# Optimization experiments

Measured on AMD Instinct MI355X. Metric: run time of the kernel, lower is better.

The kernel has to match this reference:

```python
import jax, jax.numpy as jnp
import numpy as np

N_SIDE = 7
N_NODES = N_SIDE * N_SIDE  # 49


def _grid_edge_index(h, w):
    # torch_geometric.utils.grid: 9-point stencil (8 neighbors + self-loop)
    src, dst = [], []
    for y in range(h):
        for x in range(w):
            for dy in (-1, 0, 1):
                for dx in (-1, 0, 1):
                    ny, nx = y + dy, x + dx
                    if 0 <= ny < h and 0 <= nx < w:
                        src.append(ny * w + nx)
                        dst.append(y * w + x)
    return np.stack([np.array(src), np.array(dst)]).astype(np.int64)


def _gcn_norm_adj(edge_index, n):
    # PyG GCNConv default: add self-loops (on top of any existing), weight 1,
    # deg = in-degree by edge weight, A_hat = D^-1/2 (A + I) D^-1/2
    src, dst = edge_index[0], edge_index[1]
    A = jnp.zeros((n, n), dtype=jnp.float32).at[dst, src].add(1.0)
    A = A + jnp.eye(n, dtype=jnp.float32)  # GCNConv's added self-loops
    deg = A.sum(axis=1)
    d_inv_sqrt = jnp.where(deg > 0, jax.lax.rsqrt(deg), 0.0)
    return A * d_inv_sqrt[:, None] * d_inv_sqrt[None, :]  # [n, n]


def setup_inputs() -> dict:
    key = jax.random.key(0)
    ks = jax.random.split(key, 4)
    B = 4096
    features = jax.random.normal(ks[0], (B, N_NODES, 768), dtype=jnp.float32)
    W1 = jax.random.normal(ks[1], (768, 256), dtype=jnp.float32) * (1.0 / np.sqrt(768))
    b1 = jnp.zeros((256,), dtype=jnp.float32)
    W2 = jax.random.normal(ks[2], (256, 128), dtype=jnp.float32) * (1.0 / np.sqrt(256))
    b2 = jnp.zeros((128,), dtype=jnp.float32)
    fcW = jax.random.normal(ks[3], (128, 4), dtype=jnp.float32) * (1.0 / np.sqrt(128))
    fcb = jnp.zeros((4,), dtype=jnp.float32)
    edge_index = jnp.asarray(_grid_edge_index(N_SIDE, N_SIDE))  # [2, 361]
    return {"features": features, "W1": W1, "b1": b1, "W2": W2, "b2": b2,
            "fcW": fcW, "fcb": fcb, "edge_index": edge_index}


def reference(features, W1, b1, W2, b2, fcW, fcb, edge_index):
    # features: [B, N, 768]; batched GCN over the shared 7x7 grid graph
    A_hat = _gcn_norm_adj(edge_index, N_NODES)  # [N, N]
    # GCNConv: aggregate(X @ W) + b
    h = jnp.einsum('mn,bnd->bmd', A_hat, features @ W1) + b1  # [B, N, 256]
    h = jax.nn.relu(h)
    h = jnp.einsum('mn,bnd->bmd', A_hat, h @ W2) + b2  # [B, N, 128]
    h = jax.nn.relu(h)
    pooled = h.mean(axis=1)  # [B, 128] mean over nodes
    return pooled @ fcW + fcb  # [B, 4]
```

## Files before the change

kernel.cpp:

```cpp
#include <hip/hip_runtime.h>

#define NN 49
#define D0 768
#define D1 256
#define D2 128

typedef short v8s __attribute__((ext_vector_type(8)));
typedef float v4f __attribute__((ext_vector_type(4)));
typedef int   v4i __attribute__((ext_vector_type(4)));

__device__ __forceinline__ unsigned short f2bf(float f) {
  unsigned int u = __float_as_uint(f);
  u += 0x7FFFu + ((u >> 16) & 1u);
  return (unsigned short)(u >> 16);
}
__device__ __forceinline__ float bf2f(unsigned short u) {
  return __uint_as_float((unsigned)u << 16);
}

__device__ __forceinline__ int permk(int k) {
  return (k & ~31) | ((k & 12) << 1) | ((k & 16) >> 2) | (k & 3);
}

__device__ __forceinline__ float ahat(int m, int k) {
  if (m >= NN || k >= NN) return 0.f;
  int ym = m / 7, xm = m % 7, yk = k / 7, xk = k % 7;
  int dy = ym - yk, dx = xm - xk;
  if (dy < -1 || dy > 1 || dx < -1 || dx > 1) return 0.f;
  float rm = rsqrtf((float)((1 + (ym > 0) + (ym < 6)) * (1 + (xm > 0) + (xm < 6))) + 1.0f);
  float rk = rsqrtf((float)((1 + (yk > 0) + (yk < 6)) * (1 + (xk > 0) + (xk < 6))) + 1.0f);
  return ((m == k) ? 2.0f : 1.0f) * rm * rk;
}

#define W1_IMG_BYTES 393216
#define AH_OFF       458752
#define WS_NEEDED    524288

__global__ void prep_w(const float* __restrict__ W1, const float* __restrict__ W2,
                       char* __restrict__ wimg) {
  int id = blockIdx.x * 256 + threadIdx.x;
  if (id < 24576) {
    int p = (id >> 8) & 7, tt = id & 255;
    int wvv = tt >> 6, lnn = tt & 63, qq = lnn >> 4, lmm = lnn & 15;
    int nt = p >> 1, s = p & 1;
    int n  = 64 * wvv + 16 * nt + lmm;
    int k0 = (id >> 11) * 64 + 32 * s + 4 * qq;
    v8s v;
    #pragma unroll
    for (int i = 0; i < 4; ++i) {
      v[i]     = (short)f2bf(W1[(size_t)(k0 + i) * D1 + n]);
      v[i + 4] = (short)f2bf(W1[(size_t)(k0 + 16 + i) * D1 + n]);
    }
    *(v8s*)(wimg + (size_t)id * 16) = v;
  }
  int id2 = id - 24576;
  if (id2 >= 0 && id2 < 4096) {
    int p = (id2 >> 8) & 3, tt = id2 & 255;
    int wvv = tt >> 6, lnn = tt & 63, qq = lnn >> 4, lmm = lnn & 15;
    int nt = p >> 1, s = p & 1;
    int n  = 32 * wvv + 16 * nt + lmm;
    int k0 = (id2 >> 10) * 64 + 32 * s + 4 * qq;
    v8s v;
    #pragma unroll
    for (int i = 0; i < 4; ++i) {
      v[i]     = (short)f2bf(W2[(size_t)(k0 + i) * D2 + n]);
      v[i + 4] = (short)f2bf(W2[(size_t)(k0 + 16 + i) * D2 + n]);
    }
    *(v8s*)(wimg + W1_IMG_BYTES + (size_t)id2 * 16) = v;
  }
  int id3 = id - 28672;
  if (id3 >= 0 && id3 < 2048) {
    int tt = id3 & 255, ms = id3 >> 8;
    int mt = ms >> 1, s2 = ms & 1;
    int lnn = tt & 63, qq = lnn >> 4, lmm = lnn & 15;
    int m = 16 * mt + lmm;
    v8s hi, lo;
    #pragma unroll
    for (int j = 0; j < 8; ++j) {
      int k = 32 * s2 + ((j & 4) << 2) + 4 * qq + (j & 3);
      float v = ahat(m, k);
      unsigned short h = f2bf(v);
      hi[j] = (short)h;
      lo[j] = (short)f2bf(v - bf2f(h));
    }
    *(v8s*)(wimg + AH_OFF + (size_t)id3 * 16) = hi;
    *(v8s*)(wimg + AH_OFF + 32768 + (size_t)id3 * 16) = lo;
  }
}

#define SX0    0
#define SX1    8192
#define SH1_0  16384
#define SH1_1  49152
#define SPOOL0 0
#define SPOOL1 512
#define NSMEM7 81920

__device__ __forceinline__ void ldw8(v8s* dst, const char* base) {
  #pragma unroll
  for (int p = 0; p < 8; ++p) dst[p] = *(const v8s*)(base + p * 4096);
}
__device__ __forceinline__ void ldw4(v8s* dst, const char* base) {
  #pragma unroll
  for (int p = 0; p < 4; ++p) dst[p] = *(const v8s*)(base + p * 4096);
}
__device__ __forceinline__ void commit8(char* lds, const float4& a, const float4& b) {
  v8s v;
  v[0] = (short)f2bf(a.x); v[1] = (short)f2bf(a.y);
  v[2] = (short)f2bf(a.z); v[3] = (short)f2bf(a.w);
  v[4] = (short)f2bf(b.x); v[5] = (short)f2bf(b.y);
  v[6] = (short)f2bf(b.z); v[7] = (short)f2bf(b.w);
  *(v8s*)lds = v;
}

__global__ __launch_bounds__(256, 2) void gcn_fused10(
    const float* __restrict__ X, const char* __restrict__ wimg,
    const float* __restrict__ b1v, const float* __restrict__ b2v,
    const float* __restrict__ fcWv, const float* __restrict__ fcbv,
    float* __restrict__ out)
{
  __shared__ __align__(16) char smem[NSMEM7];
  const int t  = threadIdx.x;
  const int wv = t >> 6;
  const int ln = t & 63;
  const int q  = ln >> 4;
  const int lm = ln & 15;

  if (t < 240) {
    int i = (t >= 120) ? t - 120 : t;
    int base = ((t >= 120) ? SX1 : SX0) + 6272 + i * 16;
    *(v4i*)(smem + base) = (v4i){0, 0, 0, 0};
  }

  const float* X0 = X + (size_t)(2 * blockIdx.x) * (NN * D0);
  const float* X1 = X0 + NN * D0;

  const int g1 = t + 256;
  const int b1g = (g1 >= 392) ? 1 : 0;
  const bool act3 = (t < 16);
  const int s0 = t, s1 = g1 - 392 * b1g, s2 = t + 120, s3 = t + 376;
  const int r0 = s0 >> 3, f0 = s0 & 7;
  const int r1 = s1 >> 3, f1 = s1 & 7;
  const int r2 = s2 >> 3, f2 = s2 & 7;
  const int r3 = s3 >> 3, f3 = s3 & 7;
  const float* base0 = X0 + r0 * D0 + 32 * (f0 >> 2) + 4 * (f0 & 3);
  const float* base1 = (b1g ? X1 : X0) + r1 * D0 + 32 * (f1 >> 2) + 4 * (f1 & 3);
  const float* base2 = X1 + r2 * D0 + 32 * (f2 >> 2) + 4 * (f2 & 3);
  const float* base3_ = X1 + r3 * D0 + 32 * (f3 >> 2) + 4 * (f3 & 3);
  const float* base3 = act3 ? base3_ : base0;
  const int lds0 = SX0 + ((r0 * 128 + 16 * f0) ^ ((r0 & 7) << 4));
  const int lds1 = (b1g ? SX1 : SX0) + ((r1 * 128 + 16 * f1) ^ ((r1 & 7) << 4));
  const int lds2 = SX1 + ((r2 * 128 + 16 * f2) ^ ((r2 & 7) << 4));
  const int lds3 = SX1 + (((r3 & 63) * 128 + 16 * f3) ^ ((r3 & 7) << 4));

  const int tofs = t * 16;

  v4f accA[4][4], accB[4][4];
  #pragma unroll
  for (int i = 0; i < 4; ++i)
    #pragma unroll
    for (int j = 0; j < 4; ++j) {
      accA[i][j] = (v4f){0.f, 0.f, 0.f, 0.f};
      accB[i][j] = (v4f){0.f, 0.f, 0.f, 0.f};
    }

  v8s wA[8];
  ldw8(wA, wimg + tofs);
  float4 p0a = *(const float4*)(base0);
  float4 p0b = *(const float4*)(base0 + 16);
  float4 p1a = *(const float4*)(base1);
  float4 p1b = *(const float4*)(base1 + 16);
  float4 p2a = *(const float4*)(base2);
  float4 p2b = *(const float4*)(base2 + 16);
  float4 p3a = *(const float4*)(base3);
  float4 p3b = *(const float4*)(base3 + 16);

  for (int kc = 0; kc < 12; ++kc) {
    __builtin_amdgcn_sched_barrier(0);
    __builtin_amdgcn_s_barrier();
    __builtin_amdgcn_sched_barrier(0);
    commit8((char*)smem + lds0, p0a, p0b);
    commit8((char*)smem + lds1, p1a, p1b);
    commit8((char*)smem + lds2, p2a, p2b);
    if (act3) commit8((char*)smem + lds3, p3a, p3b);
    if (kc < 11) {
      const int o = (kc + 1) * 64;
      p0a = *(const float4*)(base0 + o);
      p0b = *(const float4*)(base0 + o + 16);
      p1a = *(const float4*)(base1 + o);
      p1b = *(const float4*)(base1 + o + 16);
      p2a = *(const float4*)(base2 + o);
      p2b = *(const float4*)(base2 + o + 16);
      p3a = *(const float4*)(base3 + o);
      p3b = *(const float4*)(base3 + o + 16);
    }
    __builtin_amdgcn_sched_barrier(0);
    asm volatile("s_waitcnt lgkmcnt(0)" ::: "memory");
    __builtin_amdgcn_s_barrier();
    __builtin_amdgcn_sched_barrier(0);
    #pragma unroll
    for (int ks = 0; ks < 2; ++ks) {
      const int off = ks * 64 + (q << 4);
      v8s af[4];
      #pragma unroll
      for (int mt = 0; mt < 4; ++mt) {
        int row = mt * 16 + lm;
        af[mt] = *(const v8s*)(smem + SX0 + ((row * 128 + off) ^ ((row & 7) << 4)));
      }
      #pragma unroll
      for (int mt = 0; mt < 4; ++mt)
        #pragma unroll
        for (int nt = 0; nt < 4; ++nt)
          accA[mt][nt] = __builtin_amdgcn_mfma_f32_16x16x32_bf16(af[mt], wA[2 * nt + ks], accA[mt][nt], 0, 0, 0);
    }
    #pragma unroll
    for (int ks = 0; ks < 2; ++ks) {
      const int off = ks * 64 + (q << 4);
      v8s af[4];
      #pragma unroll
      for (int mt = 0; mt < 4; ++mt) {
        int row = mt * 16 + lm;
        af[mt] = *(const v8s*)(smem + SX1 + ((row * 128 + off) ^ ((row & 7) << 4)));
      }
      #pragma unroll
      for (int mt = 0; mt < 4; ++mt)
        #pragma unroll
        for (int nt = 0; nt < 4; ++nt)
          accB[mt][nt] = __builtin_amdgcn_mfma_f32_16x16x32_bf16(af[mt], wA[2 * nt + ks], accB[mt][nt], 0, 0, 0);
    }
    if (kc < 11) ldw8(wA, wimg + (kc + 1) * 32768 + tofs);
  }

  const char* ahimg = wimg + AH_OFF;
  v8s afH[4][2], afL[4][2];
  #pragma unroll
  for (int mt = 0; mt < 4; ++mt)
    #pragma unroll
    for (int s2 = 0; s2 < 2; ++s2) {
      const int idx = ((mt * 2 + s2) * 256 + t) * 16;
      afH[mt][s2] = *(const v8s*)(ahimg + idx);
      afL[mt][s2] = *(const v8s*)(ahimg + 32768 + idx);
    }

  v8s bA[2][4], bB[2][4];
  #pragma unroll
  for (int s2 = 0; s2 < 2; ++s2)
    #pragma unroll
    for (int nt = 0; nt < 4; ++nt) {
      v8s a, b;
      #pragma unroll
      for (int i = 0; i < 4; ++i) {
        a[i]     = (short)f2bf(accA[2 * s2][nt][i]);
        a[i + 4] = (short)f2bf(accA[2 * s2 + 1][nt][i]);
        b[i]     = (short)f2bf(accB[2 * s2][nt][i]);
        b[i + 4] = (short)f2bf(accB[2 * s2 + 1][nt][i]);
      }
      bA[s2][nt] = a; bB[s2][nt] = b;
    }

  float bi[4];
  #pragma unroll
  for (int nt = 0; nt < 4; ++nt) bi[nt] = b1v[64 * wv + 16 * nt + lm];

  #pragma unroll
  for (int bb = 0; bb < 2; ++bb) {
    v4f ag[4][4];
    #pragma unroll
    for (int mt = 0; mt < 4; ++mt)
      #pragma unroll
      for (int nt = 0; nt < 4; ++nt)
        ag[mt][nt] = (v4f){bi[nt], bi[nt], bi[nt], bi[nt]};
    #pragma unroll
    for (int s2 = 0; s2 < 2; ++s2)
      #pragma unroll
      for (int nt = 0; nt < 4; ++nt) {
        v8s b = (bb == 0) ? bA[s2][nt] : bB[s2][nt];
        #pragma unroll
        for (int mt = 0; mt < 4; ++mt) {
          ag[mt][nt] = __builtin_amdgcn_mfma_f32_16x16x32_bf16(afL[mt][s2], b, ag[mt][nt], 0, 0, 0);
          ag[mt][nt] = __builtin_amdgcn_mfma_f32_16x16x32_bf16(afH[mt][s2], b, ag[mt][nt], 0, 0, 0);
        }
      }
    const int hbase = (bb == 0) ? SH1_0 : SH1_1;
    #pragma unroll
    for (int mt = 0; mt < 4; ++mt)
      #pragma unroll
      for (int nt = 0; nt < 4; ++nt) {
        int ch  = 64 * wv + 16 * nt + lm;
        int chb = 2 * permk(ch);
        #pragma unroll
        for (int r = 0; r < 4; ++r) {
          int row = 16 * mt + 4 * q + r;
          float hv = fmaxf(ag[mt][nt][r], 0.f);
          int byte = (row * 512 + chb) ^ ((row & 7) << 4);
          *(unsigned short*)(smem + hbase + byte) = f2bf(hv);
        }
      }
  }

  const char* w2img = wimg + W1_IMG_BYTES;
  v8s w2c0[4], w2c1[4], w2c2[4], w2c3[4];
  ldw4(w2c0, w2img + tofs);
  ldw4(w2c1, w2img + 16384 + tofs);
  ldw4(w2c2, w2img + 2 * 16384 + tofs);
  ldw4(w2c3, w2img + 3 * 16384 + tofs);

  __builtin_amdgcn_sched_barrier(0);
  asm volatile("s_waitcnt lgkmcnt(0)" ::: "memory");
  __builtin_amdgcn_s_barrier();
  __builtin_amdgcn_sched_barrier(0);

  float b2i0 = b2v[32 * wv + lm];
  float b2i1 = b2v[32 * wv + 16 + lm];

  #pragma unroll
  for (int bb = 0; bb < 2; ++bb) {
    const int hbase = (bb == 0) ? SH1_0 : SH1_1;
    v4f acc3[4][2];
    #pragma unroll
    for (int i = 0; i < 4; ++i) {
      acc3[i][0] = (v4f){0.f, 0.f, 0.f, 0.f};
      acc3[i][1] = (v4f){0.f, 0.f, 0.f, 0.f};
    }
    #pragma unroll
    for (int kc = 0; kc < 4; ++kc)
      #pragma unroll
      for (int ks = 0; ks < 2; ++ks) {
        const int off = ks * 64 + (q << 4);
        v8s af[4];
        #pragma unroll
        for (int mt = 0; mt < 4; ++mt) {
          int row = mt * 16 + lm;
          int byte = (row * 512 + kc * 128 + off) ^ ((row & 7) << 4);
          af[mt] = *(const v8s*)(smem + hbase + byte);
        }
        const v8s* wc = (kc == 0) ? w2c0 : (kc == 1) ? w2c1 : (kc == 2) ? w2c2 : w2c3;
        #pragma unroll
        for (int mt = 0; mt < 4; ++mt)
          #pragma unroll
          for (int nt = 0; nt < 2; ++nt)
            acc3[mt][nt] = __builtin_amdgcn_mfma_f32_16x16x32_bf16(af[mt], wc[2 * nt + ks], acc3[mt][nt], 0, 0, 0);
      }
    v4f a2[4][2];
    #pragma unroll
    for (int mt = 0; mt < 4; ++mt) {
      a2[mt][0] = (v4f){b2i0, b2i0, b2i0, b2i0};
      a2[mt][1] = (v4f){b2i1, b2i1, b2i1, b2i1};
    }
    #pragma unroll
    for (int s2 = 0; s2 < 2; ++s2)
      #pragma unroll
      for (int nt = 0; nt < 2; ++nt) {
        v8s b;
        #pragma unroll
        for (int i = 0; i < 4; ++i) {
          b[i]     = (short)f2bf(acc3[2 * s2][nt][i]);
          b[i + 4] = (short)f2bf(acc3[2 * s2 + 1][nt][i]);
        }
        #pragma unroll
        for (int mt = 0; mt < 4; ++mt) {
          a2[mt][nt] = __builtin_amdgcn_mfma_f32_16x16x32_bf16(afL[mt][s2], b, a2[mt][nt], 0, 0, 0);
          a2[mt][nt] = __builtin_amdgcn_mfma_f32_16x16x32_bf16(afH[mt][s2], b, a2[mt][nt], 0, 0, 0);
        }
      }
    float ps0 = 0.f, ps1 = 0.f;
    #pragma unroll
    for (int mt = 0; mt < 3; ++mt)
      #pragma unroll
      for (int r = 0; r < 4; ++r) {
        ps0 += fmaxf(a2[mt][0][r], 0.f);
        ps1 += fmaxf(a2[mt][1][r], 0.f);
      }
    if (q == 0) {
      ps0 += fmaxf(a2[3][0][0], 0.f);
      ps1 += fmaxf(a2[3][1][0], 0.f);
    }
    ps0 += __shfl_xor(ps0, 16); ps0 += __shfl_xor(ps0, 32);
    ps1 += __shfl_xor(ps1, 16); ps1 += __shfl_xor(ps1, 32);
    float* spool = (float*)(smem + ((bb == 0) ? SPOOL0 : SPOOL1));
    if (q == 0) {
      spool[32 * wv + lm]      = ps0 * (1.0f / 49.0f);
      spool[32 * wv + 16 + lm] = ps1 * (1.0f / 49.0f);
    }
  }
  __syncthreads();
  {
    const int bb = wv >> 1;
    const int c0 = (wv & 1) * 2;
    const float* spool = (const float*)(smem + (bb ? SPOOL1 : SPOOL0));
    float d0 = spool[ln];
    float d1 = spool[ln + 64];
    float a0 = d0 * fcWv[ln * 4 + c0]     + d1 * fcWv[(ln + 64) * 4 + c0];
    float a1 = d0 * fcWv[ln * 4 + c0 + 1] + d1 * fcWv[(ln + 64) * 4 + c0 + 1];
    #pragma unroll
    for (int s = 32; s; s >>= 1) { a0 += __shfl_xor(a0, s); a1 += __shfl_xor(a1, s); }
    if (ln == 0) {
      out[(size_t)(2 * blockIdx.x + bb) * 4 + c0]     = a0 + fcbv[c0];
      out[(size_t)(2 * blockIdx.x + bb) * 4 + c0 + 1] = a1 + fcbv[c0 + 1];
    }
  }
}

#define OFF_SX    0
#define OFF_SWT   8192
#define OFF_SC    0
#define OFF_SWT2  0
#define OFF_SPOOL 25872
#define OFF_SPF   30096
#define OFF_SH1   40960
#define OFF_NBRW  73728
#define OFF_NBRI  75492
#define OFF_B1    77256
#define OFF_B2    78280
#define OFF_FCW   78792
#define OFF_FCB   80840
#define SMEM_SZ   80856

__global__ __launch_bounds__(256, 2) void gcn_fused_fb(
    const float* __restrict__ X, const float* __restrict__ W1,
    const float* __restrict__ b1v, const float* __restrict__ W2,
    const float* __restrict__ b2v, const float* __restrict__ fcWv,
    const float* __restrict__ fcbv, float* __restrict__ out)
{
  __shared__ __align__(16) char smem[SMEM_SZ];
  const int t  = threadIdx.x;
  const int wv = t >> 6;
  const int ln = t & 63;
  const int q  = ln >> 4;
  const int lm = ln & 15;

  float* nbrW = (float*)(smem + OFF_NBRW);
  int*   nbrI = (int*)  (smem + OFF_NBRI);
  float* b1s  = (float*)(smem + OFF_B1);
  float* b2s  = (float*)(smem + OFF_B2);
  float* fcWs = (float*)(smem + OFF_FCW);
  float* fcbs = (float*)(smem + OFF_FCB);
  float* sC   = (float*)(smem + OFF_SC);

  if (t < D1) b1s[t] = b1v[t];
  if (t < D2) b2s[t] = b2v[t];
  fcWs[t]       = fcWv[t];
  fcWs[t + 256] = fcWv[t + 256];
  if (t < 4) fcbs[t] = fcbv[t];
  if (t < NN) {
    int y = t / 7, x = t % 7;
    float rm = rsqrtf((float)((1 + (y > 0) + (y < 6)) * (1 + (x > 0) + (x < 6))) + 1.0f);
    int cnt = 0;
    for (int dy = -1; dy <= 1; ++dy)
      for (int dx = -1; dx <= 1; ++dx) {
        int ny = y + dy, nx = x + dx;
        if (ny >= 0 && ny < 7 && nx >= 0 && nx < 7) {
          int n = ny * 7 + nx;
          float rn = rsqrtf((float)((1 + (ny > 0) + (ny < 6)) * (1 + (nx > 0) + (nx < 6))) + 1.0f);
          nbrW[t * 9 + cnt] = ((n == t) ? 2.0f : 1.0f) * rm * rn;
          nbrI[t * 9 + cnt] = n;
          ++cnt;
        }
      }
    for (; cnt < 9; ++cnt) { nbrW[t * 9 + cnt] = 0.0f; nbrI[t * 9 + cnt] = 0; }
  }
  __syncthreads();

  const float* Xb = X + (size_t)blockIdx.x * (NN * D0);
  v4f acc[4][4];
  #pragma unroll
  for (int i = 0; i < 4; ++i)
    #pragma unroll
    for (int j = 0; j < 4; ++j)
      acc[i][j] = (v4f){0.f, 0.f, 0.f, 0.f};

  for (int kc = 0; kc < 12; ++kc) {
    __syncthreads();
    #pragma unroll
    for (int p = 0; p < 4; ++p) {
      int idx = t + 256 * p;
      int row = idx >> 4;
      int k4  = (idx & 15) << 2;
      float4 v = {0.f, 0.f, 0.f, 0.f};
      if (row < NN) v = *(const float4*)(Xb + row * D0 + kc * 64 + k4);
      ushort4 s;
      s.x = f2bf(v.x); s.y = f2bf(v.y); s.z = f2bf(v.z); s.w = f2bf(v.w);
      int byte = row * 128 + 2 * permk(k4);
      byte ^= (row & 7) << 4;
      *(ushort4*)(smem + OFF_SX + byte) = s;
    }
    #pragma unroll
    for (int p = 0; p < 4; ++p) {
      int bid2 = t + 256 * p;
      int k0 = (bid2 & 15) << 2;
      int n0 = (bid2 >> 4) << 2;
      const float* wp = W1 + (size_t)(kc * 64 + k0) * D1 + n0;
      float4 r0 = *(const float4*)(wp);
      float4 r1 = *(const float4*)(wp + D1);
      float4 r2 = *(const float4*)(wp + 2 * D1);
      float4 r3 = *(const float4*)(wp + 3 * D1);
      int kb = 2 * permk(k0);
      ushort4 s; int byte;
      s.x = f2bf(r0.x); s.y = f2bf(r1.x); s.z = f2bf(r2.x); s.w = f2bf(r3.x);
      byte = (n0 + 0) * 128 + kb; byte ^= ((n0 + 0) & 7) << 4;
      *(ushort4*)(smem + OFF_SWT + byte) = s;
      s.x = f2bf(r0.y); s.y = f2bf(r1.y); s.z = f2bf(r2.y); s.w = f2bf(r3.y);
      byte = (n0 + 1) * 128 + kb; byte ^= ((n0 + 1) & 7) << 4;
      *(ushort4*)(smem + OFF_SWT + byte) = s;
      s.x = f2bf(r0.z); s.y = f2bf(r1.z); s.z = f2bf(r2.z); s.w = f2bf(r3.z);
      byte = (n0 + 2) * 128 + kb; byte ^= ((n0 + 2) & 7) << 4;
      *(ushort4*)(smem + OFF_SWT + byte) = s;
      s.x = f2bf(r0.w); s.y = f2bf(r1.w); s.z = f2bf(r2.w); s.w = f2bf(r3.w);
      byte = (n0 + 3) * 128 + kb; byte ^= ((n0 + 3) & 7) << 4;
      *(ushort4*)(smem + OFF_SWT + byte) = s;
    }
    __syncthreads();
    #pragma unroll
    for (int ks = 0; ks < 2; ++ks) {
      int off = ks * 64 + (q << 4);
      v8s af[4], bf[4];
      #pragma unroll
      for (int mt = 0; mt < 4; ++mt) {
        int row = mt * 16 + lm;
        int byte = row * 128 + off; byte ^= (row & 7) << 4;
        af[mt] = *(const v8s*)(smem + OFF_SX + byte);
      }
      #pragma unroll
      for (int nt = 0; nt < 4; ++nt) {
        int n = (wv * 4 + nt) * 16 + lm;
        int byte = n * 128 + off; byte ^= (n & 7) << 4;
        bf[nt] = *(const v8s*)(smem + OFF_SWT + byte);
      }
      #pragma unroll
      for (int mt = 0; mt < 4; ++mt)
        #pragma unroll
        for (int nt = 0; nt < 4; ++nt)
          acc[mt][nt] = __builtin_amdgcn_mfma_f32_16x16x32_bf16(af[mt], bf[nt], acc[mt][nt], 0, 0, 0);
    }
  }

  #pragma unroll
  for (int h = 0; h < 2; ++h) {
    __syncthreads();
    if ((wv >> 1) == h) {
      #pragma unroll
      for (int mt = 0; mt < 4; ++mt) {
        int rbase = mt * 16 + (q << 2);
        #pragma unroll
        for (int nt = 0; nt < 4; ++nt) {
          int c = ((wv & 1) * 4 + nt) * 16 + lm;
          #pragma unroll
          for (int r = 0; r < 4; ++r) {
            int row = rbase + r;
            if (row < NN) sC[row * 132 + c] = acc[mt][nt][r];
          }
        }
      }
    }
    __syncthreads();
    for (int p = 0; p < 7; ++p) {
      int idx = t + 256 * p;
      if (idx < NN * 32) {
        int m  = idx >> 5;
        int d4 = (idx & 31) << 2;
        int dg = h * 128 + d4;
        float a0 = b1s[dg], a1 = b1s[dg + 1], a2 = b1s[dg + 2], a3 = b1s[dg + 3];
        #pragma unroll
        for (int e = 0; e < 9; ++e) {
          float w = nbrW[m * 9 + e];
          int   n = nbrI[m * 9 + e];
          float4 cv = *(const float4*)(sC + n * 132 + d4);
          a0 += w * cv.x; a1 += w * cv.y; a2 += w * cv.z; a3 += w * cv.w;
        }
        a0 = fmaxf(a0, 0.f); a1 = fmaxf(a1, 0.f); a2 = fmaxf(a2, 0.f); a3 = fmaxf(a3, 0.f);
        ushort4 s; s.x = f2bf(a0); s.y = f2bf(a1); s.z = f2bf(a2); s.w = f2bf(a3);
        int byte = m * 512 + 2 * permk(dg);
        byte ^= (m & 7) << 4;
        *(ushort4*)(smem + OFF_SH1 + byte) = s;
      }
    }
  }

  v4f acc2[4][2];
  #pragma unroll
  for (int i = 0; i < 4; ++i) { acc2[i][0] = (v4f){0.f,0.f,0.f,0.f}; acc2[i][1] = (v4f){0.f,0.f,0.f,0.f}; }

  for (int kc = 0; kc < 4; ++kc) {
    __syncthreads();
    #pragma unroll
    for (int p = 0; p < 2; ++p) {
      int bid2 = t + 256 * p;
      int k0 = (bid2 & 15) << 2;
      int n0 = (bid2 >> 4) << 2;
      const float* wp = W2 + (size_t)(kc * 64 + k0) * D2 + n0;
      float4 r0 = *(const float4*)(wp);
      float4 r1 = *(const float4*)(wp + D2);
      float4 r2 = *(const float4*)(wp + 2 * D2);
      float4 r3 = *(const float4*)(wp + 3 * D2);
      int kb = 2 * permk(k0);
      ushort4 s; int byte;
      s.x = f2bf(r0.x); s.y = f2bf(r1.x); s.z = f2bf(r2.x); s.w = f2bf(r3.x);
      byte = (n0 + 0) * 128 + kb; byte ^= ((n0 + 0) & 7) << 4;
      *(ushort4*)(smem + OFF_SWT2 + byte) = s;
      s.x = f2bf(r0.y); s.y = f2bf(r1.y); s.z = f2bf(r2.y); s.w = f2bf(r3.y);
      byte = (n0 + 1) * 128 + kb; byte ^= ((n0 + 1) & 7) << 4;
      *(ushort4*)(smem + OFF_SWT2 + byte) = s;
      s.x = f2bf(r0.z); s.y = f2bf(r1.z); s.z = f2bf(r2.z); s.w = f2bf(r3.z);
      byte = (n0 + 2) * 128 + kb; byte ^= ((n0 + 2) & 7) << 4;
      *(ushort4*)(smem + OFF_SWT2 + byte) = s;
      s.x = f2bf(r0.w); s.y = f2bf(r1.w); s.z = f2bf(r2.w); s.w = f2bf(r3.w);
      byte = (n0 + 3) * 128 + kb; byte ^= ((n0 + 3) & 7) << 4;
      *(ushort4*)(smem + OFF_SWT2 + byte) = s;
    }
    __syncthreads();
    #pragma unroll
    for (int ks = 0; ks < 2; ++ks) {
      int off = ks * 64 + (q << 4);
      v8s af[4], bf2[2];
      #pragma unroll
      for (int mt = 0; mt < 4; ++mt) {
        int row = mt * 16 + lm;
        int byte = row * 512 + kc * 128 + off; byte ^= (row & 7) << 4;
        af[mt] = *(const v8s*)(smem + OFF_SH1 + byte);
      }
      #pragma unroll
      for (int nt = 0; nt < 2; ++nt) {
        int n = (wv * 2 + nt) * 16 + lm;
        int byte = n * 128 + off; byte ^= (n & 7) << 4;
        bf2[nt] = *(const v8s*)(smem + OFF_SWT2 + byte);
      }
      #pragma unroll
      for (int mt = 0; mt < 4; ++mt)
        #pragma unroll
        for (int nt = 0; nt < 2; ++nt)
          acc2[mt][nt] = __builtin_amdgcn_mfma_f32_16x16x32_bf16(af[mt], bf2[nt], acc2[mt][nt], 0, 0, 0);
    }
  }

  __syncthreads();
  #pragma unroll
  for (int mt = 0; mt < 4; ++mt) {
    int rbase = mt * 16 + (q << 2);
    #pragma unroll
    for (int nt = 0; nt < 2; ++nt) {
      int c = (wv * 2 + nt) * 16 + lm;
      #pragma unroll
      for (int r = 0; r < 4; ++r) {
        int row = rbase + r;
        if (row < NN) sC[row * 132 + c] = acc2[mt][nt][r];
      }
    }
  }
  __syncthreads();
  {
    int d4 = (t & 31) << 2;
    int g  = t >> 5;
    float p0 = 0.f, p1 = 0.f, p2 = 0.f, p3 = 0.f;
    int m0 = g * 7, m1 = (g * 7 + 7 < NN) ? (g * 7 + 7) : NN;
    for (int m = m0; m < m1; ++m) {
      float a0 = b2s[d4], a1 = b2s[d4 + 1], a2 = b2s[d4 + 2], a3 = b2s[d4 + 3];
      #pragma unroll
      for (int e = 0; e < 9; ++e) {
        float w = nbrW[m * 9 + e];
        int   n = nbrI[m * 9 + e];
        float4 cv = *(const float4*)(sC + n * 132 + d4);
        a0 += w * cv.x; a1 += w * cv.y; a2 += w * cv.z; a3 += w * cv.w;
      }
      p0 += fmaxf(a0, 0.f); p1 += fmaxf(a1, 0.f); p2 += fmaxf(a2, 0.f); p3 += fmaxf(a3, 0.f);
    }
    float* sp = (float*)(smem + OFF_SPOOL) + g * 132 + d4;
    sp[0] = p0; sp[1] = p1; sp[2] = p2; sp[3] = p3;
  }
  __syncthreads();
  if (t < D2) {
    const float* sp = (const float*)(smem + OFF_SPOOL);
    float s = 0.f;
    #pragma unroll
    for (int g = 0; g < 8; ++g) s += sp[g * 132 + t];
    ((float*)(smem + OFF_SPF))[t] = s * (1.0f / 49.0f);
  }
  __syncthreads();
  if (t < 4) {
    const float* pf = (const float*)(smem + OFF_SPF);
    float a = fcbs[t];
    for (int d = 0; d < D2; ++d) a += pf[d] * fcWs[d * 4 + t];
    out[(size_t)blockIdx.x * 4 + t] = a;
  }
}

extern "C" void kernel_launch(void* const* d_in, const int* in_sizes, int n_in,
                              void* d_out, int out_size, void* d_ws, size_t ws_size,
                              hipStream_t stream) {
  const float* X   = (const float*)d_in[0];
  const float* W1  = (const float*)d_in[1];
  const float* b1  = (const float*)d_in[2];
  const float* W2  = (const float*)d_in[3];
  const float* b2  = (const float*)d_in[4];
  const float* fcW = (const float*)d_in[5];
  const float* fcb = (const float*)d_in[6];
  float* out = (float*)d_out;
  int B = in_sizes[0] / (NN * D0);
  if (d_ws != nullptr && ws_size >= (size_t)WS_NEEDED && (B % 2) == 0) {
    prep_w<<<120, 256, 0, stream>>>(W1, W2, (char*)d_ws);
    gcn_fused10<<<B / 2, 256, 0, stream>>>(X, (const char*)d_ws, b1, b2, fcW, fcb, out);
  } else {
    gcn_fused_fb<<<B, 256, 0, stream>>>(X, W1, b1, W2, b2, fcW, fcb, out);
  }
}
```

Before: 182.9 us.

## Double-buffer X tiles in LDS and overlap with MFMA, shrink LDS footprint

Converts the layer-1 K-loop from a single LDS buffer with two barriers per iteration into a ping-pong double buffer. MFMAs now run on one buffer while the next chunk is committed to the other, leaving one barrier per iteration. The layout is also repacked so the H1 and pool regions overlap the X staging area, cutting LDS from 80KB to 65KB per block. That should help two blocks per CU fit more comfortably, but the register-held prefetch now runs two chunks ahead, which adds register pressure.

```diff
diff --git a/kernel.cpp b/kernel.cpp
--- a/kernel.cpp
+++ b/kernel.cpp
@@ -88,13 +88,13 @@
   }
 }
 
-#define SX0    0
-#define SX1    8192
-#define SH1_0  16384
-#define SH1_1  49152
-#define SPOOL0 0
-#define SPOOL1 512
-#define NSMEM7 81920
+#define SXP    16384
+#define SXB    8192
+#define SH1_0  0
+#define SH1_1  32768
+#define SPOOL0 65536
+#define SPOOL1 66048
+#define NSMEM11 66560
 
 __device__ __forceinline__ void ldw8(v8s* dst, const char* base) {
   #pragma unroll
@@ -113,23 +113,23 @@
   *(v8s*)lds = v;
 }
 
-__global__ __launch_bounds__(256, 2) void gcn_fused10(
+__global__ __launch_bounds__(256, 2) void gcn_fused11(
     const float* __restrict__ X, const char* __restrict__ wimg,
     const float* __restrict__ b1v, const float* __restrict__ b2v,
     const float* __restrict__ fcWv, const float* __restrict__ fcbv,
     float* __restrict__ out)
 {
-  __shared__ __align__(16) char smem[NSMEM7];
+  __shared__ __align__(16) char smem[NSMEM11];
   const int t  = threadIdx.x;
   const int wv = t >> 6;
   const int ln = t & 63;
   const int q  = ln >> 4;
   const int lm = ln & 15;
 
-  if (t < 240) {
-    int i = (t >= 120) ? t - 120 : t;
-    int base = ((t >= 120) ? SX1 : SX0) + 6272 + i * 16;
-    *(v4i*)(smem + base) = (v4i){0, 0, 0, 0};
+  if (t < 120) {
+    #pragma unroll
+    for (int b = 0; b < 4; ++b)
+      *(v4i*)(smem + b * 8192 + 6272 + t * 16) = (v4i){0, 0, 0, 0};
   }
 
   const float* X0 = X + (size_t)(2 * blockIdx.x) * (NN * D0);
@@ -148,10 +148,10 @@
   const float* base2 = X1 + r2 * D0 + 32 * (f2 >> 2) + 4 * (f2 & 3);
   const float* base3_ = X1 + r3 * D0 + 32 * (f3 >> 2) + 4 * (f3 & 3);
   const float* base3 = act3 ? base3_ : base0;
-  const int lds0 = SX0 + ((r0 * 128 + 16 * f0) ^ ((r0 & 7) << 4));
-  const int lds1 = (b1g ? SX1 : SX0) + ((r1 * 128 + 16 * f1) ^ ((r1 & 7) << 4));
-  const int lds2 = SX1 + ((r2 * 128 + 16 * f2) ^ ((r2 & 7) << 4));
-  const int lds3 = SX1 + (((r3 & 63) * 128 + 16 * f3) ^ ((r3 & 7) << 4));
+  const int lds0 = ((r0 * 128 + 16 * f0) ^ ((r0 & 7) << 4));
+  const int lds1 = b1g * SXB + ((r1 * 128 + 16 * f1) ^ ((r1 & 7) << 4));
+  const int lds2 = SXB + ((r2 * 128 + 16 * f2) ^ ((r2 & 7) << 4));
+  const int lds3 = SXB + (((r3 & 63) * 128 + 16 * f3) ^ ((r3 & 7) << 4));
 
   const int tofs = t * 16;
 
@@ -175,60 +175,80 @@
   float4 p3a = *(const float4*)(base3);
   float4 p3b = *(const float4*)(base3 + 16);
 
+  commit8((char*)smem + lds0, p0a, p0b);
+  commit8((char*)smem + lds1, p1a, p1b);
+  commit8((char*)smem + lds2, p2a, p2b);
+  if (act3) commit8((char*)smem + lds3, p3a, p3b);
+  {
+    p0a = *(const float4*)(base0 + 64);
+    p0b = *(const float4*)(base0 + 64 + 16);
+    p1a = *(const float4*)(base1 + 64);
+    p1b = *(const float4*)(base1 + 64 + 16);
+    p2a = *(const float4*)(base2 + 64);
+    p2b = *(const float4*)(base2 + 64 + 16);
+    p3a = *(const float4*)(base3 + 64);
+    p3b = *(const float4*)(base3 + 64 + 16);
+  }
+  __builtin_amdgcn_sched_barrier(0);
+  asm volatile("s_waitcnt lgkmcnt(0)" ::: "memory");
+  __builtin_amdgcn_s_barrier();
+  __builtin_amdgcn_sched_barrier(0);
+
   for (int kc = 0; kc < 12; ++kc) {
-    __builtin_amdgcn_sched_barrier(0);
-    __builtin_amdgcn_s_barrier();
-    __builtin_amdgcn_sched_barrier(0);
-    commit8((char*)smem + lds0, p0a, p0b);
-    commit8((char*)smem + lds1, p1a, p1b);
-    commit8((char*)smem + lds2, p2a, p2b);
-    if (act3) commit8((char*)smem + lds3, p3a, p3b);
+    const int pb = (kc & 1) * SXP;
+    const int cb = ((kc + 1) & 1) * SXP;
+    #pragma unroll
+    for (int ks = 0; ks < 2; ++ks) {
+      const int off = ks * 64 + (q << 4);
+      v8s af[4];
+      #pragma unroll
+      for (int mt = 0; mt < 4; ++mt) {
+        int row = mt * 16 + lm;
+        af[mt] = *(const v8s*)(smem + pb + ((row * 128 + off) ^ ((row & 7) << 4)));
+      }
+      #pragma unroll
+      for (int mt = 0; mt < 4; ++mt)
+        #pragma unroll
+        for (int nt = 0; nt < 4; ++nt)
+          accA[mt][nt] = __builtin_amdgcn_mfma_f32_16x16x32_bf16(af[mt], wA[2 * nt + ks], accA[mt][nt], 0, 0, 0);
+    }
+    #pragma unroll
+    for (int ks = 0; ks < 2; ++ks) {
+      const int off = ks * 64 + (q << 4);
+      v8s af[4];
+      #pragma unroll
+      for (int mt = 0; mt < 4; ++mt) {
+        int row = mt * 16 + lm;
+        af[mt] = *(const v8s*)(smem + pb + SXB + ((row * 128 + off) ^ ((row & 7) << 4)));
+      }
+      #pragma unroll
+      for (int mt = 0; mt < 4; ++mt)
+        #pragma unroll
+        for (int nt = 0; nt < 4; ++nt)
+          accB[mt][nt] = __builtin_amdgcn_mfma_f32_16x16x32_bf16(af[mt], wA[2 * nt + ks], accB[mt][nt], 0, 0, 0);
+    }
     if (kc < 11) {
-      const int o = (kc + 1) * 64;
-      p0a = *(const float4*)(base0 + o);
-      p0b = *(const float4*)(base0 + o + 16);
-      p1a = *(const float4*)(base1 + o);
-      p1b = *(const float4*)(base1 + o + 16);
-      p2a = *(const float4*)(base2 + o);
-      p2b = *(const float4*)(base2 + o + 16);
-      p3a = *(const float4*)(base3 + o);
-      p3b = *(const float4*)(base3 + o + 16);
+      ldw8(wA, wimg + (kc + 1) * 32768 + tofs);
+      commit8((char*)smem + cb + lds0, p0a, p0b);
+      commit8((char*)smem + cb + lds1, p1a, p1b);
+      commit8((char*)smem + cb + lds2, p2a, p2b);
+      if (act3) commit8((char*)smem + cb + lds3, p3a, p3b);
+      if (kc < 10) {
+        const int o = (kc + 2) * 64;
+        p0a = *(const float4*)(base0 + o);
+        p0b = *(const float4*)(base0 + o + 16);
+        p1a = *(const float4*)(base1 + o);
+        p1b = *(const float4*)(base1 + o + 16);
+        p2a = *(const float4*)(base2 + o);
+        p2b = *(const float4*)(base2 + o + 16);
+        p3a = *(const float4*)(base3 + o);
+        p3b = *(const float4*)(base3 + o + 16);
+      }
     }
     __builtin_amdgcn_sched_barrier(0);
     asm volatile("s_waitcnt lgkmcnt(0)" ::: "memory");
     __builtin_amdgcn_s_barrier();
     __builtin_amdgcn_sched_barrier(0);
-    #pragma unroll
-    for (int ks = 0; ks < 2; ++ks) {
-      const int off = ks * 64 + (q << 4);
-      v8s af[4];
-      #pragma unroll
-      for (int mt = 0; mt < 4; ++mt) {
-        int row = mt * 16 + lm;
-        af[mt] = *(const v8s*)(smem + SX0 + ((row * 128 + off) ^ ((row & 7) << 4)));
-      }
-      #pragma unroll
-      for (int mt = 0; mt < 4; ++mt)
-        #pragma unroll
-        for (int nt = 0; nt < 4; ++nt)
-          accA[mt][nt] = __builtin_amdgcn_mfma_f32_16x16x32_bf16(af[mt], wA[2 * nt + ks], accA[mt][nt], 0, 0, 0);
-    }
-    #pragma unroll
-    for (int ks = 0; ks < 2; ++ks) {
-      const int off = ks * 64 + (q << 4);
-      v8s af[4];
-      #pragma unroll
-      for (int mt = 0; mt < 4; ++mt) {
-        int row = mt * 16 + lm;
-        af[mt] = *(const v8s*)(smem + SX1 + ((row * 128 + off) ^ ((row & 7) << 4)));
-      }
-      #pragma unroll
-      for (int mt = 0; mt < 4; ++mt)
-        #pragma unroll
-        for (int nt = 0; nt < 4; ++nt)
-          accB[mt][nt] = __builtin_amdgcn_mfma_f32_16x16x32_bf16(af[mt], wA[2 * nt + ks], accB[mt][nt], 0, 0, 0);
-    }
-    if (kc < 11) ldw8(wA, wimg + (kc + 1) * 32768 + tofs);
   }
 
   const char* ahimg = wimg + AH_OFF;
@@ -697,7 +717,7 @@
   int B = in_sizes[0] / (NN * D0);
   if (d_ws != nullptr && ws_size >= (size_t)WS_NEEDED && (B % 2) == 0) {
     prep_w<<<120, 256, 0, stream>>>(W1, W2, (char*)d_ws);
-    gcn_fused10<<<B / 2, 256, 0, stream>>>(X, (const char*)d_ws, b1, b2, fcW, fcb, out);
+    gcn_fused11<<<B / 2, 256, 0, stream>>>(X, (const char*)d_ws, b1, b2, fcW, fcb, out);
   } else {
     gcn_fused_fb<<<B, 256, 0, stream>>>(X, W1, b1, W2, b2, fcW, fcb, out);
   }
```

New measurement: 180.1 us. No clear change (-1.5%).
